# Optimization experiments

Measured on AMD Instinct MI355X. Metric: run time of the kernel, lower is better.

The kernel has to match this reference:

```python
import jax, jax.numpy as jnp
import numpy as np

HEADS = 8
GS = 16
C = 512
E = 512
SCALE = (E / HEADS) ** -0.5
PNAMES = ['sa_qkv_w','sa_qkv_b','sa_pa_w','sa_pa_b','sa_ln1_g','sa_ln1_b','sa_f1_w','sa_f1_b','sa_f2_w','sa_f2_b','sa_ln2_g','sa_ln2_b','sa_c1_w','sa_c1_b','sa_c2_w','sa_c2_b','sa_bn_g','sa_bn_b','ca_q_w','ca_q_b','ca_k_w','ca_k_b','ca_v_w','ca_v_b','ca_pa_w','ca_pa_b','p_q_w','p_q_b','p_k_w','p_k_b','p_v_w','p_v_b','p_pa_w','p_pa_b','p_ln_g','p_ln_b','p_lin_w','p_lin_b']


def _ln(x, g, b, eps=1e-5):
    m = x.mean(-1, keepdims=True)
    v = jnp.var(x, axis=-1, keepdims=True)
    return (x - m) / jnp.sqrt(v + eps) * g + b


def _conv1x1(x, w, b):
    return jnp.einsum('bchw,oc->bohw', x, w) + b[None, :, None, None]


def _up_ac(x, out=GS):
    # bilinear upsample, align_corners=True (nn.UpsamplingBilinear2d)
    H = x.shape[2]
    pos = jnp.arange(out) * (H - 1) / (out - 1)
    lo = jnp.floor(pos).astype(jnp.int32)
    hi = jnp.minimum(lo + 1, H - 1)
    w = (pos - lo).astype(x.dtype)
    xr = x[:, :, lo, :] * (1 - w)[None, None, :, None] + x[:, :, hi, :] * w[None, None, :, None]
    return xr[:, :, :, lo] * (1 - w) + xr[:, :, :, hi] * w


def _asri(x, p):
    # Sequence_ASRI: GAP tokens -> attention over the batch axis -> pixel-shuffle back
    B = x.shape[0]; ch = E // HEADS
    gap = x.mean((2, 3))                                             # [B,C]
    qkv = (gap @ p['sa_qkv_w'].T + p['sa_qkv_b']).reshape(B, 4, ch, HEADS).transpose(1, 3, 0, 2)  # [4,H,B,ch]
    q, k, v, skip = qkv[0], qkv[1], qkv[2], qkv[3]
    attn = jax.nn.softmax(jnp.einsum('hbc,hdc->hbd', q, k) * SCALE, -1)  # [H,B,B]
    o = jnp.einsum('hbd,hdc->hbc', attn, v)
    merge = lambda t: t.transpose(1, 2, 0).reshape(B, E)             # 'head b c -> b (c head)'
    a = merge(o) @ p['sa_pa_w'].T + p['sa_pa_b'] + merge(skip)
    h = jax.nn.relu(_ln(a, p['sa_ln1_g'], p['sa_ln1_b']) @ p['sa_f1_w'].T + p['sa_f1_b'])
    a = h @ p['sa_f2_w'].T + p['sa_f2_b'] + a
    s = _ln(a, p['sa_ln2_g'], p['sa_ln2_b']) @ p['sa_c1_w'].T + p['sa_c1_b']  # [B,C*16]
    s = _up_ac(s.reshape(B, C, 4, 4))                                 # pixel shuffle p1=p2=4 then bilinear to 16x16
    s = _conv1x1(s, p['sa_c2_w'], p['sa_c2_b'])
    # BatchNorm2d in eval mode (running_mean=0, running_var=1, eps=1e-5)
    s = s / np.float32(np.sqrt(1.0 + 1e-5)) * p['sa_bn_g'][None, :, None, None] + p['sa_bn_b'][None, :, None, None]
    return x + jax.nn.relu(s)


def _sscm(x1, x2, p):
    # Sequence_SSCM: GAP-token q/k over batch axis, full spatial v
    B = x1.shape[0]; ch = E // HEADS
    q = (x1.mean((2, 3)) @ p['ca_q_w'].T + p['ca_q_b']).reshape(B, ch, HEADS).transpose(2, 0, 1)  # [H,B,ch]
    k = (x2.mean((2, 3)) @ p['ca_k_w'].T + p['ca_k_b']).reshape(B, ch, HEADS).transpose(2, 0, 1)
    v = _conv1x1(x2, p['ca_v_w'], p['ca_v_b']).reshape(B, ch, HEADS, GS, GS).transpose(2, 0, 1, 3, 4).reshape(HEADS, B, ch * GS * GS)
    attn = jax.nn.softmax(jnp.einsum('hbc,hdc->hbd', q, k) * SCALE, -1)  # [H,B,B]
    o = jnp.einsum('hbd,hdm->hbm', attn, v)
    o = o.reshape(HEADS, B, ch, GS, GS).transpose(1, 2, 0, 3, 4).reshape(B, E, GS, GS)
    return jax.nn.relu(_conv1x1(o, p['ca_pa_w'], p['ca_pa_b']))


def _pixel(x1, x2, p):
    # Pixel_SSCM: pixel-wise cross-batch attention (no scale -- matches source)
    B = x1.shape[0]; ch = E // HEADS; N = GS * GS
    split = lambda t: t.reshape(B, ch, HEADS, N).transpose(2, 0, 3, 1)   # 'b (c head) h w -> head b (h w) c'
    q = split(_conv1x1(x1, p['p_q_w'], p['p_q_b']))                      # [H,B,N,ch]
    k = split(_conv1x1(x2, p['p_k_w'], p['p_k_b']))
    v = split(_conv1x1(x2, p['p_v_w'], p['p_v_b'])).reshape(HEADS, B * N, ch)
    attn = jax.nn.softmax(jnp.einsum('hbnc,hqmc->hbqnm', q, k), -1)      # [H,B,B,N,N]
    attn = attn.transpose(1, 0, 3, 2, 4).reshape(B, HEADS, N, B * N)     # 'head b q h w -> b head h (q w)'
    o = jnp.einsum('bhnm,hmc->bhnc', attn, v)
    o = o.transpose(0, 3, 1, 2).reshape(B, E, GS, GS)                    # 'b head (h w) c -> b (c head) h w'
    o = _conv1x1(o, p['p_pa_w'], p['p_pa_b']) + x1
    t = o.reshape(B, C, N).transpose(0, 2, 1)                            # [B,N,C]
    t = jax.nn.relu(_ln(t, p['p_ln_g'], p['p_ln_b']) @ p['p_lin_w'].T + p['p_lin_b'])
    return t.transpose(0, 2, 1).reshape(B, C, GS, GS)


def _hrlm(p, xs, xq):
    sa_s = _asri(xs, p)
    sa_q = _asri(xq, p)
    ca_s = _sscm(sa_s, sa_q, p)
    ca_q = _sscm(sa_q, sa_s, p)
    return _pixel(sa_s, ca_q, p), _pixel(sa_q, ca_s, p)


def setup_inputs():
    key = jax.random.key(0)
    ks = iter(jax.random.split(key, 64))
    w = lambda *s: (jax.random.normal(next(ks), s) * 0.02).astype(jnp.float32)
    z = lambda n: jnp.zeros((n,), jnp.float32)
    o = lambda n: jnp.ones((n,), jnp.float32)
    return dict(
        fea_support=jax.random.normal(next(ks), (8, C, GS, GS), jnp.float32),
        fea_query=jax.random.normal(next(ks), (8, C, GS, GS), jnp.float32),
        sa_qkv_w=w(4 * E, C), sa_qkv_b=z(4 * E),
        sa_pa_w=w(E, E), sa_pa_b=z(E),
        sa_ln1_g=o(E), sa_ln1_b=z(E),
        sa_f1_w=w(E, E), sa_f1_b=z(E), sa_f2_w=w(E, E), sa_f2_b=z(E),
        sa_ln2_g=o(E), sa_ln2_b=z(E),
        sa_c1_w=w(C * 16, E), sa_c1_b=z(C * 16),
        sa_c2_w=w(C, E), sa_c2_b=z(C),
        sa_bn_g=o(C), sa_bn_b=z(C),
        ca_q_w=w(E, C), ca_q_b=z(E), ca_k_w=w(E, C), ca_k_b=z(E),
        ca_v_w=w(E, C), ca_v_b=z(E), ca_pa_w=w(C, E), ca_pa_b=z(C),
        p_q_w=w(E, C), p_q_b=z(E), p_k_w=w(E, C), p_k_b=z(E),
        p_v_w=w(E, C), p_v_b=z(E), p_pa_w=w(C, E), p_pa_b=z(C),
        p_ln_g=o(C), p_ln_b=z(C), p_lin_w=w(C, C), p_lin_b=z(C),
    )


def reference(fea_support, fea_query, sa_qkv_w, sa_qkv_b, sa_pa_w, sa_pa_b, sa_ln1_g, sa_ln1_b, sa_f1_w, sa_f1_b, sa_f2_w, sa_f2_b, sa_ln2_g, sa_ln2_b, sa_c1_w, sa_c1_b, sa_c2_w, sa_c2_b, sa_bn_g, sa_bn_b, ca_q_w, ca_q_b, ca_k_w, ca_k_b, ca_v_w, ca_v_b, ca_pa_w, ca_pa_b, p_q_w, p_q_b, p_k_w, p_k_b, p_v_w, p_v_b, p_pa_w, p_pa_b, p_ln_g, p_ln_b, p_lin_w, p_lin_b):
    p = dict(zip(PNAMES, (sa_qkv_w, sa_qkv_b, sa_pa_w, sa_pa_b, sa_ln1_g, sa_ln1_b, sa_f1_w, sa_f1_b, sa_f2_w, sa_f2_b, sa_ln2_g, sa_ln2_b, sa_c1_w, sa_c1_b, sa_c2_w, sa_c2_b, sa_bn_g, sa_bn_b, ca_q_w, ca_q_b, ca_k_w, ca_k_b, ca_v_w, ca_v_b, ca_pa_w, ca_pa_b, p_q_w, p_q_b, p_k_w, p_k_b, p_v_w, p_v_b, p_pa_w, p_pa_b, p_ln_g, p_ln_b, p_lin_w, p_lin_b)))
    return _hrlm(p, fea_support, fea_query)
```

## Files before the change

### kernel.cpp

```cpp
#include <hip/hip_runtime.h>
#include <cmath>

#define IMG 131072
#define BIGF 1048576

#define CF_RELU  1
#define CF_RES   2
#define CF_BN    4
#define CF_SPLIT 8
#define CF_TRANS 16

typedef __attribute__((ext_vector_type(8))) short short8;
typedef __attribute__((ext_vector_type(4))) short short4v;
typedef __attribute__((ext_vector_type(4))) float f32x4;

__device__ __forceinline__ float wave_sum(float v){
    #pragma unroll
    for (int off = 32; off; off >>= 1) v += __shfl_xor(v, off);
    return v;
}

__device__ __forceinline__ unsigned short bf16_rn(float x){
    union { float f; unsigned u; } v; v.f = x;
    unsigned r = v.u + 0x7FFF + ((v.u >> 16) & 1);
    return (unsigned short)(r >> 16);
}
__device__ __forceinline__ float bf16_to_f(unsigned short h){
    union { float f; unsigned u; } v; v.u = ((unsigned)h) << 16;
    return v.f;
}
__device__ __forceinline__ unsigned pack_split(float x){
    unsigned short hi = bf16_rn(x);
    unsigned short lo = bf16_rn(x - bf16_to_f(hi));
    return (unsigned)hi | ((unsigned)lo << 16);
}
__device__ __forceinline__ unsigned pk_hi(unsigned a, unsigned b){
    return __builtin_amdgcn_perm(b, a, 0x05040100u);
}
__device__ __forceinline__ unsigned pk_lo(unsigned a, unsigned b){
    return __builtin_amdgcn_perm(b, a, 0x07060302u);
}

struct GapJobs  { const float* x[2]; float* o[2]; };
struct G8Job    { const float* in; const float* W; const float* bias; const float* add; float* out; };
struct G8Jobs   { G8Job j[4]; };
struct AAJobs   { const float* qkv[2]; float* om[2]; };
struct LnJobs   { const float* in[2]; float* out[2]; };
struct UpJobs   { const float* in[2]; float* out[2]; };
struct SAJobs   { const float* q8[2]; const float* k8[2]; float* aw[2]; };
struct SPJobs   { const float* aw[2]; const float* v[2]; float* out[2]; };
struct ZJobs    { float* p[2]; };
struct ConvJob  { const float* X; const float* X2; const float* W; const float* B; const float* R;
                  const float* bng; const float* bnb; float* O; int flags; };
struct ConvJobs { ConvJob j[6]; };
struct PixJob   { const unsigned* Q; const unsigned* K; const unsigned* V; float* Oa; float* Ob; };
struct PixJobs  { PixJob j[2]; };

__global__ __launch_bounds__(64) void k_gap(GapJobs jo){
    const int br = blockIdx.y;
    const int bc = blockIdx.x;
    const int lane = threadIdx.x;
    const float* p = jo.x[br] + (size_t)bc * 256;
    float s = p[lane] + p[lane + 64] + p[lane + 128] + p[lane + 192];
    s = wave_sum(s);
    if (lane == 0) jo.o[br][bc] = s * (1.0f / 256.0f);
}

__global__ __launch_bounds__(64) void k_gemm8(G8Jobs jo, int add_off, int add_stride, int O, int relu){
    const G8Job j = jo.j[blockIdx.y];
    const int o = blockIdx.x;
    const int lane = threadIdx.x;
    const float* wr = j.W + (size_t)o * 512;
    float acc[8] = {0,0,0,0,0,0,0,0};
    #pragma unroll
    for (int i = 0; i < 8; i++){
        float w = wr[lane + 64*i];
        #pragma unroll
        for (int b = 0; b < 8; b++) acc[b] += w * j.in[b*512 + lane + 64*i];
    }
    #pragma unroll
    for (int b = 0; b < 8; b++) acc[b] = wave_sum(acc[b]);
    if (lane < 8){
        float v = acc[0];
        #pragma unroll
        for (int b = 1; b < 8; b++) if (lane == b) v = acc[b];
        v += j.bias[o];
        if (j.add) v += j.add[lane*add_stride + add_off + o];
        if (relu) v = fmaxf(v, 0.f);
        j.out[(size_t)lane * O + o] = v;
    }
}

__global__ __launch_bounds__(64) void k_asri_attn(AAJobs jo){
    const int br = blockIdx.y;
    const float* qkv = jo.qkv[br];
    const int h = blockIdx.x >> 3, b = blockIdx.x & 7, c = threadIdx.x;
    const int ci = c*8 + h;
    float qc = qkv[b*2048 + ci];
    float s[8];
    #pragma unroll
    for (int d = 0; d < 8; d++){
        float p = qc * qkv[d*2048 + 512 + ci];
        p = wave_sum(p);
        s[d] = p * 0.125f;
    }
    float m = s[0];
    #pragma unroll
    for (int d = 1; d < 8; d++) m = fmaxf(m, s[d]);
    float sum = 0.f;
    #pragma unroll
    for (int d = 0; d < 8; d++){ s[d] = __expf(s[d]-m); sum += s[d]; }
    float r = 1.f / sum;
    float oc = 0.f;
    #pragma unroll
    for (int d = 0; d < 8; d++) oc += s[d]*r * qkv[d*2048 + 1024 + ci];
    jo.om[br][b*512 + ci] = oc;
}

__global__ __launch_bounds__(64) void k_ln8(LnJobs jo,
    const float* __restrict__ g, const float* __restrict__ be)
{
    const int br = blockIdx.y;
    const int b = blockIdx.x, lane = threadIdx.x;
    const float* in = jo.in[br];
    float v[8]; float s = 0.f;
    #pragma unroll
    for (int i = 0; i < 8; i++){ v[i] = in[b*512 + lane + 64*i]; s += v[i]; }
    s = wave_sum(s);
    float mean = s * (1.f/512.f);
    float q = 0.f;
    #pragma unroll
    for (int i = 0; i < 8; i++){ float d = v[i]-mean; q += d*d; }
    q = wave_sum(q);
    float rstd = rsqrtf(q*(1.f/512.f) + 1e-5f);
    #pragma unroll
    for (int i = 0; i < 8; i++){
        int c = lane + 64*i;
        jo.out[br][b*512 + c] = (v[i]-mean)*rstd*g[c] + be[c];
    }
}

__global__ __launch_bounds__(256) void k_up(UpJobs jo){
    const int br = blockIdx.y;
    const int idx = blockIdx.x*256 + threadIdx.x;
    const int x = idx & 15, y = (idx >> 4) & 15, bc = idx >> 8;
    float px = (float)(x*3) / 15.0f, py = (float)(y*3) / 15.0f;
    int lx = (int)px, ly = (int)py;
    float wx = px - lx, wy = py - ly;
    int hx = min(lx+1, 3), hy = min(ly+1, 3);
    const float* p = jo.in[br] + (size_t)bc * 16;
    float v00 = p[ly*4+lx], v01 = p[ly*4+hx], v10 = p[hy*4+lx], v11 = p[hy*4+hx];
    float a0 = v00*(1.f-wy) + v10*wy;
    float a1 = v01*(1.f-wy) + v11*wy;
    jo.out[br][idx] = a0*(1.f-wx) + a1*wx;
}

__global__ __launch_bounds__(256) void k_zero(ZJobs jo){
    jo.p[blockIdx.y][(size_t)blockIdx.x*256 + threadIdx.x] = 0.f;
}

#define LDK 40
__device__ __forceinline__ void convm_body(
    const float* __restrict__ Xb, const float* __restrict__ X2b,
    const float* __restrict__ W,
    const float* __restrict__ bias, const float* __restrict__ resb,
    const float* __restrict__ bng, const float* __restrict__ bnb, float bninv,
    float* __restrict__ outb, int flags, int o0, int n0, unsigned short* lds)
{
    const int tid512 = threadIdx.x;
    const int g   = tid512 >> 8;
    const int tid = tid512 & 255;
    unsigned short* sAh = lds + g*10240;
    unsigned short* sAl = sAh + 2560;
    unsigned short* sBh = sAl + 2560;
    unsigned short* sBl = sBh + 2560;
    const int wv = tid >> 6, lane = tid & 63;
    const int quad = lane >> 4, l16 = lane & 15;
    const int wo = (wv >> 1) * 32, wn = (wv & 1) * 32;
    const int so  = tid >> 2, sk8 = (tid & 3) * 8;
    const int sp  = tid & 15, sn  = (tid >> 4) * 4;

    const bool trans = (flags & CF_TRANS) != 0;
    int so_g = o0 + so;
    if (trans) so_g = ((so_g & 63) << 3) | (so_g >> 6);

    const float* wrow = W + (size_t)so_g*512 + g*256 + sk8;
    const size_t xoff = (size_t)(g*256 + 2*sp)*256 + n0 + sn;
    const float* xrow  = Xb + xoff;
    const float* x2row = X2b ? X2b + xoff : nullptr;

    auto ldx4 = [&](size_t off){
        float4 v = *(const float4*)(xrow + off);
        if (x2row){
            float4 w2 = *(const float4*)(x2row + off);
            v.x += w2.x; v.y += w2.y; v.z += w2.z; v.w += w2.w;
        }
        return v;
    };

    f32x4 acc[2][2] = {};
    float4 a0 = *(const float4*)(wrow);
    float4 a1 = *(const float4*)(wrow + 4);
    float4 x0 = ldx4(0);
    float4 x1 = ldx4(256);

    for (int k0 = 0; k0 < 256; k0 += 32){
        __syncthreads();
        {
            float wa[8] = {a0.x,a0.y,a0.z,a0.w,a1.x,a1.y,a1.z,a1.w};
            #pragma unroll
            for (int j = 0; j < 4; j++){
                unsigned short h0 = bf16_rn(wa[2*j]);
                unsigned short h1 = bf16_rn(wa[2*j+1]);
                unsigned short g0 = bf16_rn(wa[2*j]   - bf16_to_f(h0));
                unsigned short g1 = bf16_rn(wa[2*j+1] - bf16_to_f(h1));
                *(unsigned*)&sAh[so*LDK + sk8 + 2*j] = (unsigned)h0 | ((unsigned)h1 << 16);
                *(unsigned*)&sAl[so*LDK + sk8 + 2*j] = (unsigned)g0 | ((unsigned)g1 << 16);
            }
            float xe[4] = {x0.x,x0.y,x0.z,x0.w};
            float xo[4] = {x1.x,x1.y,x1.z,x1.w};
            #pragma unroll
            for (int j = 0; j < 4; j++){
                unsigned short h0 = bf16_rn(xe[j]);
                unsigned short h1 = bf16_rn(xo[j]);
                unsigned short g0 = bf16_rn(xe[j] - bf16_to_f(h0));
                unsigned short g1 = bf16_rn(xo[j] - bf16_to_f(h1));
                *(unsigned*)&sBh[(sn+j)*LDK + 2*sp] = (unsigned)h0 | ((unsigned)h1 << 16);
                *(unsigned*)&sBl[(sn+j)*LDK + 2*sp] = (unsigned)g0 | ((unsigned)g1 << 16);
            }
        }
        __syncthreads();
        if (k0 + 32 < 256){
            a0 = *(const float4*)(wrow + k0 + 32);
            a1 = *(const float4*)(wrow + k0 + 36);
            x0 = ldx4((size_t)(k0+32)*256);
            x1 = ldx4((size_t)(k0+32)*256 + 256);
        }
        short8 ah[2], al[2], bh[2], bl[2];
        #pragma unroll
        for (int t = 0; t < 2; t++){
            int ai = (wo + 16*t + l16)*LDK + quad*8;
            ah[t] = *(const short8*)&sAh[ai];
            al[t] = *(const short8*)&sAl[ai];
            int bi = (wn + 16*t + l16)*LDK + quad*8;
            bh[t] = *(const short8*)&sBh[bi];
            bl[t] = *(const short8*)&sBl[bi];
        }
        if (trans){
            #pragma unroll
            for (int mt = 0; mt < 2; mt++){
                #pragma unroll
                for (int nt = 0; nt < 2; nt++){
                    acc[mt][nt] = __builtin_amdgcn_mfma_f32_16x16x32_bf16(bh[nt], ah[mt], acc[mt][nt], 0, 0, 0);
                    acc[mt][nt] = __builtin_amdgcn_mfma_f32_16x16x32_bf16(bl[nt], ah[mt], acc[mt][nt], 0, 0, 0);
                    acc[mt][nt] = __builtin_amdgcn_mfma_f32_16x16x32_bf16(bh[nt], al[mt], acc[mt][nt], 0, 0, 0);
                }
            }
        } else {
            #pragma unroll
            for (int mt = 0; mt < 2; mt++){
                #pragma unroll
                for (int nt = 0; nt < 2; nt++){
                    acc[mt][nt] = __builtin_amdgcn_mfma_f32_16x16x32_bf16(ah[mt], bh[nt], acc[mt][nt], 0, 0, 0);
                    acc[mt][nt] = __builtin_amdgcn_mfma_f32_16x16x32_bf16(ah[mt], bl[nt], acc[mt][nt], 0, 0, 0);
                    acc[mt][nt] = __builtin_amdgcn_mfma_f32_16x16x32_bf16(al[mt], bh[nt], acc[mt][nt], 0, 0, 0);
                }
            }
        }
    }
    __syncthreads();
    float* red = (float*)lds;
    if (g == 1){
        float* r = red + tid*20;
        #pragma unroll
        for (int mt = 0; mt < 2; mt++)
            #pragma unroll
            for (int nt = 0; nt < 2; nt++)
                *(f32x4*)(r + (mt*2+nt)*4) = acc[mt][nt];
    }
    __syncthreads();
    if (g == 0){
        float* r = red + tid*20;
        #pragma unroll
        for (int mt = 0; mt < 2; mt++)
            #pragma unroll
            for (int nt = 0; nt < 2; nt++){
                f32x4 o4 = *(const f32x4*)(r + (mt*2+nt)*4);
                acc[mt][nt] += o4;
            }
        if (trans){
            unsigned* op = (unsigned*)outb;
            #pragma unroll
            for (int mt = 0; mt < 2; mt++){
                #pragma unroll
                for (int nt = 0; nt < 2; nt++){
                    const int p  = o0 + wo + 16*mt + l16;
                    const int nb = n0 + wn + 16*nt + quad*4;
                    const int osrc = ((p & 63) << 3) | (p >> 6);
                    const float bs = bias[osrc];
                    #pragma unroll
                    for (int rr = 0; rr < 4; rr++){
                        float v = acc[mt][nt][rr] + bs;
                        op[(size_t)(nb+rr)*512 + p] = pack_split(v);
                    }
                }
            }
        } else {
            #pragma unroll
            for (int mt = 0; mt < 2; mt++){
                #pragma unroll
                for (int nt = 0; nt < 2; nt++){
                    const int n  = n0 + wn + 16*nt + l16;
                    const int ob = o0 + wo + 16*mt + quad*4;
                    #pragma unroll
                    for (int rr = 0; rr < 4; rr++){
                        const int o = ob + rr;
                        float v = acc[mt][nt][rr] + bias[o];
                        if (flags & CF_BN)   v = v*(bninv*bng[o]) + bnb[o];
                        if (flags & CF_RELU) v = fmaxf(v, 0.f);
                        if (flags & CF_RES)  v += resb[(size_t)o*256 + n];
                        if (flags & CF_SPLIT){
                            ((unsigned*)outb)[(size_t)o*256 + n] = pack_split(v);
                        } else {
                            outb[(size_t)o*256 + n] = v;
                        }
                    }
                }
            }
        }
    }
}

__global__ __launch_bounds__(512) void k_convm(ConvJobs jo, float bninv)
{
    __shared__ unsigned short lds[20480];
    const int z = blockIdx.z;
    const ConvJob j = jo.j[z >> 3];
    const int b = z & 7;
    convm_body(j.X + (size_t)b*IMG,
               j.X2 ? j.X2 + (size_t)b*IMG : nullptr,
               j.W, j.B,
               j.R ? j.R + (size_t)b*IMG : nullptr,
               j.bng, j.bnb, bninv,
               j.O + (size_t)b*IMG, j.flags,
               blockIdx.y*64, blockIdx.x*64, lds);
}

__global__ __launch_bounds__(64) void k_sscm_attn(SAJobs jo)
{
    const int br = blockIdx.y;
    const int h = blockIdx.x >> 3, b = blockIdx.x & 7, c = threadIdx.x;
    const int ci = c*8 + h;
    float qc = jo.q8[br][b*512 + ci];
    float s[8];
    #pragma unroll
    for (int d = 0; d < 8; d++){
        float p = qc * jo.k8[br][d*512 + ci];
        p = wave_sum(p);
        s[d] = p * 0.125f;
    }
    float m = s[0];
    #pragma unroll
    for (int d = 1; d < 8; d++) m = fmaxf(m, s[d]);
    float sum = 0.f;
    #pragma unroll
    for (int d = 0; d < 8; d++){ s[d] = __expf(s[d]-m); sum += s[d]; }
    float r = 1.f/sum;
    if (c < 8){
        float v = s[0];
        #pragma unroll
        for (int d = 1; d < 8; d++) if (c == d) v = s[d];
        jo.aw[br][blockIdx.x*8 + c] = v*r;
    }
}

__global__ __launch_bounds__(256) void k_sscm_apply(SPJobs jo)
{
    const int br = blockIdx.y;
    const int idx = blockIdx.x*256 + threadIdx.x;
    const int pix = idx & 255, e = (idx >> 8) & 511, b = idx >> 17;
    const int h = e & 7;
    const float* aw = jo.aw[br] + (h*8 + b)*8;
    const float* v = jo.v[br];
    float acc = 0.f;
    #pragma unroll
    for (int d = 0; d < 8; d++) acc += aw[d] * v[(size_t)d*IMG + (size_t)e*256 + pix];
    jo.out[br][idx] = acc;
}

__global__ __launch_bounds__(256) void k_pixel_mfma(PixJobs jo)
{
    __shared__ char smem[40960];
    unsigned short* sQh = (unsigned short*)smem;
    unsigned short* sQl = sQh + 2*64*40;
    unsigned short* sKh = sQl + 2*64*40;
    unsigned short* sKl = sKh + 2*64*40;
    unsigned short* sP  = (unsigned short*)smem;
    unsigned short* sVh = sKh;
    unsigned short* sVl = sKl;

    const int br = blockIdx.y >> 3, b = blockIdx.y & 7;
    const PixJob J = jo.j[br];
    const int nt = blockIdx.x & 3, dg = blockIdx.x >> 2;
    const int h = blockIdx.z;
    const int tid = threadIdx.x;
    const int wv = tid >> 6, lane = tid & 63;
    const int quad = lane >> 4, l16 = lane & 15;
    const int n0 = nt * 64;

    {
        const unsigned* Qt = J.Q + (size_t)b*IMG + (size_t)n0*512 + h*64;
        const int q = tid >> 2, i0 = (tid & 3) * 16;
        const unsigned* src = Qt + (size_t)q*512 + i0;
        uint4 w0 = *(const uint4*)(src);
        uint4 w1 = *(const uint4*)(src + 4);
        uint4 w2 = *(const uint4*)(src + 8);
        uint4 w3 = *(const uint4*)(src + 12);
        unsigned hb[8], lb[8];
        hb[0]=pk_hi(w0.x,w0.y); hb[1]=pk_hi(w0.z,w0.w); hb[2]=pk_hi(w1.x,w1.y); hb[3]=pk_hi(w1.z,w1.w);
        hb[4]=pk_hi(w2.x,w2.y); hb[5]=pk_hi(w2.z,w2.w); hb[6]=pk_hi(w3.x,w3.y); hb[7]=pk_hi(w3.z,w3.w);
        lb[0]=pk_lo(w0.x,w0.y); lb[1]=pk_lo(w0.z,w0.w); lb[2]=pk_lo(w1.x,w1.y); lb[3]=pk_lo(w1.z,w1.w);
        lb[4]=pk_lo(w2.x,w2.y); lb[5]=pk_lo(w2.z,w2.w); lb[6]=pk_lo(w3.x,w3.y); lb[7]=pk_lo(w3.z,w3.w);
        int dst = (i0>>5)*2560 + q*40 + (i0&31);
        *(uint4*)&sQh[dst]     = *(uint4*)&hb[0];
        *(uint4*)&sQh[dst + 8] = *(uint4*)&hb[4];
        *(uint4*)&sQl[dst]     = *(uint4*)&lb[0];
        *(uint4*)&sQl[dst + 8] = *(uint4*)&lb[4];
    }
    __syncthreads();

    short8 bqh[2], bql[2];
    #pragma unroll
    for (int ks = 0; ks < 2; ks++){
        int idx = ks*2560 + (wv*16 + l16)*40 + quad*8;
        bqh[ks] = *(const short8*)&sQh[idx];
        bql[ks] = *(const short8*)&sQl[idx];
    }

    f32x4 oac[4] = {};

    for (int dd = 0; dd < 4; dd++){
        const int d = dg*4 + dd;

        f32x4 S[16] = {};
        #pragma unroll
        for (int mq = 0; mq < 4; mq++){
            if (mq | dd) __syncthreads();
            {
                const unsigned* Kt = J.K + (size_t)d*IMG + (size_t)(mq*64)*512 + h*64;
                const int mloc = tid & 63, cb0 = tid >> 6;
                #pragma unroll
                for (int p = 0; p < 2; p++){
                    int cb = cb0 + 4*p;
                    const unsigned* src = Kt + (size_t)mloc*512 + cb*8;
                    uint4 wa = *(const uint4*)(src);
                    uint4 wb = *(const uint4*)(src + 4);
                    union { short8 s; unsigned u[4]; } hu, lu;
                    hu.u[0]=pk_hi(wa.x,wa.y); hu.u[1]=pk_hi(wa.z,wa.w);
                    hu.u[2]=pk_hi(wb.x,wb.y); hu.u[3]=pk_hi(wb.z,wb.w);
                    lu.u[0]=pk_lo(wa.x,wa.y); lu.u[1]=pk_lo(wa.z,wa.w);
                    lu.u[2]=pk_lo(wb.x,wb.y); lu.u[3]=pk_lo(wb.z,wb.w);
                    int idx = (cb>>2)*2560 + mloc*40 + (cb&3)*8;
                    *(short8*)&sKh[idx] = hu.s;
                    *(short8*)&sKl[idx] = lu.s;
                }
            }
            __syncthreads();
            #pragma unroll
            for (int mtl = 0; mtl < 4; mtl++){
                int t = mq*4 + mtl;
                #pragma unroll
                for (int ks = 0; ks < 2; ks++){
                    int idx = ks*2560 + (mtl*16 + l16)*40 + quad*8;
                    short8 ah = *(const short8*)&sKh[idx];
                    short8 al = *(const short8*)&sKl[idx];
                    S[t] = __builtin_amdgcn_mfma_f32_16x16x32_bf16(ah, bqh[ks], S[t], 0, 0, 0);
                    S[t] = __builtin_amdgcn_mfma_f32_16x16x32_bf16(ah, bql[ks], S[t], 0, 0, 0);
                    S[t] = __builtin_amdgcn_mfma_f32_16x16x32_bf16(al, bqh[ks], S[t], 0, 0, 0);
                }
            }
        }

        {
            float mx = -3.4e38f;
            #pragma unroll
            for (int t = 0; t < 16; t++)
                #pragma unroll
                for (int r = 0; r < 4; r++) mx = fmaxf(mx, S[t][r]);
            mx = fmaxf(mx, __shfl_xor(mx, 16));
            mx = fmaxf(mx, __shfl_xor(mx, 32));
            float sum = 0.f;
            #pragma unroll
            for (int t = 0; t < 16; t++)
                #pragma unroll
                for (int r = 0; r < 4; r++){ S[t][r] = __expf(S[t][r]-mx); sum += S[t][r]; }
            sum += __shfl_xor(sum, 16);
            sum += __shfl_xor(sum, 32);
            float rr = 1.f/sum;
            #pragma unroll
            for (int t = 0; t < 16; t++)
                #pragma unroll
                for (int r = 0; r < 4; r++) S[t][r] *= rr;
        }

        #pragma unroll
        for (int hm = 0; hm < 2; hm++){
            __syncthreads();
            #pragma unroll
            for (int mtl = 0; mtl < 8; mtl++){
                int t = hm*8 + mtl;
                short4v p4;
                #pragma unroll
                for (int r = 0; r < 4; r++) p4[r] = (short)bf16_rn(S[t][r]);
                int idx = (mtl>>1)*2560 + (wv*16 + l16)*40 + 16*(mtl&1) + quad*4;
                *(short4v*)&sP[idx] = p4;
            }
            #pragma unroll
            for (int sub = 0; sub < 2; sub++){
                if (sub) __syncthreads();
                {
                    const unsigned* Vp = J.V + (size_t)d*IMG + (size_t)h*256 + hm*128 + sub*64;
                    const int mp = tid & 31, c0 = tid >> 5;
                    #pragma unroll
                    for (int p = 0; p < 8; p++){
                        int c = c0 + 8*p;
                        const unsigned* src = Vp + (size_t)c*2048 + 2*mp;
                        uint2 w = *(const uint2*)(src);
                        int idx = ((2*mp)>>5)*2560 + c*40 + ((2*mp)&31);
                        *(unsigned*)&sVh[idx] = pk_hi(w.x, w.y);
                        *(unsigned*)&sVl[idx] = pk_lo(w.x, w.y);
                    }
                }
                __syncthreads();
                #pragma unroll
                for (int l = 0; l < 2; l++){
                    int gks = sub*2 + l;
                    int pidx = gks*2560 + (wv*16 + l16)*40 + quad*8;
                    short8 bp = *(const short8*)&sP[pidx];
                    #pragma unroll
                    for (int ct = 0; ct < 4; ct++){
                        int vidx = l*2560 + (ct*16 + l16)*40 + quad*8;
                        short8 vh = *(const short8*)&sVh[vidx];
                        short8 vl = *(const short8*)&sVl[vidx];
                        oac[ct] = __builtin_amdgcn_mfma_f32_16x16x32_bf16(vh, bp, oac[ct], 0, 0, 0);
                        oac[ct] = __builtin_amdgcn_mfma_f32_16x16x32_bf16(vl, bp, oac[ct], 0, 0, 0);
                    }
                }
            }
        }
    }

    {
        float* base = (J.Ob ? (dg ? J.Ob : J.Oa) : J.Oa);
        float* Obp = base + (size_t)b * IMG;
        const int q = n0 + wv*16 + l16;
        if (J.Ob){
            #pragma unroll
            for (int ct = 0; ct < 4; ct++){
                #pragma unroll
                for (int r = 0; r < 4; r++){
                    int c = ct*16 + quad*4 + r;
                    Obp[(size_t)(c*8+h)*256 + q] = oac[ct][r];
                }
            }
        } else {
            #pragma unroll
            for (int ct = 0; ct < 4; ct++){
                #pragma unroll
                for (int r = 0; r < 4; r++){
                    int c = ct*16 + quad*4 + r;
                    unsafeAtomicAdd(&Obp[(size_t)(c*8+h)*256 + q], oac[ct][r]);
                }
            }
        }
    }
}

__global__ __launch_bounds__(64) void k_ln_pix(LnJobs jo,
    const float* __restrict__ g, const float* __restrict__ be)
{
    const int br = blockIdx.y;
    const int bn = blockIdx.x;
    const int b = bn >> 8, n = bn & 255;
    const int lane = threadIdx.x;
    const float* p = jo.in[br] + (size_t)b*IMG + n;
    float v[8]; float s = 0.f;
    #pragma unroll
    for (int i = 0; i < 8; i++){ v[i] = p[(size_t)(lane + 64*i)*256]; s += v[i]; }
    s = wave_sum(s);
    float mean = s * (1.f/512.f);
    float q = 0.f;
    #pragma unroll
    for (int i = 0; i < 8; i++){ float d = v[i]-mean; q += d*d; }
    q = wave_sum(q);
    float rstd = rsqrtf(q*(1.f/512.f) + 1e-5f);
    #pragma unroll
    for (int i = 0; i < 8; i++){
        int c = lane + 64*i;
        jo.out[br][(size_t)b*IMG + (size_t)c*256 + n] = (v[i]-mean)*rstd*g[c] + be[c];
    }
}

extern "C" void kernel_launch(void* const* d_in, const int* in_sizes, int n_in,
                              void* d_out, int out_size, void* d_ws, size_t ws_size,
                              hipStream_t stream)
{
    const float* xs    = (const float*)d_in[0];
    const float* xq    = (const float*)d_in[1];
    const float* qkvw  = (const float*)d_in[2];  const float* qkvb = (const float*)d_in[3];
    const float* paw   = (const float*)d_in[4];  const float* pab  = (const float*)d_in[5];
    const float* ln1g  = (const float*)d_in[6];  const float* ln1b = (const float*)d_in[7];
    const float* f1w   = (const float*)d_in[8];  const float* f1b  = (const float*)d_in[9];
    const float* f2w   = (const float*)d_in[10]; const float* f2b  = (const float*)d_in[11];
    const float* ln2g  = (const float*)d_in[12]; const float* ln2b = (const float*)d_in[13];
    const float* c1w   = (const float*)d_in[14]; const float* c1b  = (const float*)d_in[15];
    const float* c2w   = (const float*)d_in[16]; const float* c2b  = (const float*)d_in[17];
    const float* bng   = (const float*)d_in[18]; const float* bnb  = (const float*)d_in[19];
    const float* caqw  = (const float*)d_in[20]; const float* caqb = (const float*)d_in[21];
    const float* cakw  = (const float*)d_in[22]; const float* cakb = (const float*)d_in[23];
    const float* cavw  = (const float*)d_in[24]; const float* cavb = (const float*)d_in[25];
    const float* capw  = (const float*)d_in[26]; const float* capb = (const float*)d_in[27];
    const float* pqw   = (const float*)d_in[28]; const float* pqb  = (const float*)d_in[29];
    const float* pkw   = (const float*)d_in[30]; const float* pkb  = (const float*)d_in[31];
    const float* pvw   = (const float*)d_in[32]; const float* pvb  = (const float*)d_in[33];
    const float* ppw   = (const float*)d_in[34]; const float* ppb  = (const float*)d_in[35];
    const float* plng  = (const float*)d_in[36]; const float* plnb = (const float*)d_in[37];
    const float* plinw = (const float*)d_in[38]; const float* plinb= (const float*)d_in[39];

    const size_t SMF = 262144;
    float* ws = (float*)d_ws;
    float* smb = ws;
    float* B[14];
    for (int i = 0; i < 14; i++) B[i] = ws + SMF + (size_t)i*BIGF;
    float* sa_s = B[0]; float* sa_q = B[1];
    float* ca_s = B[2]; float* ca_q = B[3];
    const bool paired_pixel = ws_size >= (SMF + 12*(size_t)BIGF)*sizeof(float) + 1024;
    const bool has_dsplit   = ws_size >= (SMF + 14*(size_t)BIGF)*sizeof(float) + 1024;

    auto SM = [&](int br){ return smb + (size_t)br*131072; };
    auto GAP=[&](int br){ return SM(br); };            auto QKV=[&](int br){ return SM(br)+4096; };
    auto OM =[&](int br){ return SM(br)+20480; };      auto AA =[&](int br){ return SM(br)+24576; };
    auto HB =[&](int br){ return SM(br)+28672; };      auto A2 =[&](int br){ return SM(br)+32768; };
    auto LNB=[&](int br){ return SM(br)+36864; };      auto S8 =[&](int br){ return SM(br)+40960; };
    auto ATW=[&](int br){ return SM(br)+106496; };     auto Q8 =[&](int br){ return SM(br)+107008; };
    auto K8 =[&](int br){ return SM(br)+111104; };

    const float bninv = 1.0f / sqrtf(1.0f + 1e-5f);
    float* out0 = (float*)d_out;
    float* out1 = out0 + (size_t)BIGF;

    {
        GapJobs gj = {{xs, xq}, {GAP(0), GAP(1)}};
        k_gap<<<dim3(4096,2), 64, 0, stream>>>(gj);
        G8Jobs qj = {{{GAP(0), qkvw, qkvb, nullptr, QKV(0)}, {GAP(1), qkvw, qkvb, nullptr, QKV(1)}}};
        k_gemm8<<<dim3(2048,2), 64, 0, stream>>>(qj, 0, 0, 2048, 0);
        AAJobs aj = {{QKV(0), QKV(1)}, {OM(0), OM(1)}};
        k_asri_attn<<<dim3(64,2), 64, 0, stream>>>(aj);
        G8Jobs pj = {{{OM(0), paw, pab, QKV(0), AA(0)}, {OM(1), paw, pab, QKV(1), AA(1)}}};
        k_gemm8<<<dim3(512,2), 64, 0, stream>>>(pj, 1536, 2048, 512, 0);
        LnJobs l1 = {{AA(0), AA(1)}, {LNB(0), LNB(1)}};
        k_ln8<<<dim3(8,2), 64, 0, stream>>>(l1, ln1g, ln1b);
        G8Jobs fj = {{{LNB(0), f1w, f1b, nullptr, HB(0)}, {LNB(1), f1w, f1b, nullptr, HB(1)}}};
        k_gemm8<<<dim3(512,2), 64, 0, stream>>>(fj, 0, 0, 512, 1);
        G8Jobs f2j = {{{HB(0), f2w, f2b, AA(0), A2(0)}, {HB(1), f2w, f2b, AA(1), A2(1)}}};
        k_gemm8<<<dim3(512,2), 64, 0, stream>>>(f2j, 0, 512, 512, 0);
        LnJobs l2 = {{A2(0), A2(1)}, {LNB(0), LNB(1)}};
        k_ln8<<<dim3(8,2), 64, 0, stream>>>(l2, ln2g, ln2b);
        G8Jobs cj = {{{LNB(0), c1w, c1b, nullptr, S8(0)}, {LNB(1), c1w, c1b, nullptr, S8(1)}}};
        k_gemm8<<<dim3(8192,2), 64, 0, stream>>>(cj, 0, 0, 8192, 0);
        UpJobs uj = {{S8(0), S8(1)}, {B[4], B[5]}};
        k_up<<<dim3(4096,2), 256, 0, stream>>>(uj);
        ConvJobs c2j = {};
        c2j.j[0] = {B[4], nullptr, c2w, c2b, xs, bng, bnb, sa_s, CF_BN|CF_RELU|CF_RES};
        c2j.j[1] = {B[5], nullptr, c2w, c2b, xq, bng, bnb, sa_q, CF_BN|CF_RELU|CF_RES};
        k_convm<<<dim3(4,8,16), 512, 0, stream>>>(c2j, bninv);
    }

    {
        GapJobs gj = {{sa_s, sa_q}, {GAP(0), GAP(1)}};
        k_gap<<<dim3(4096,2), 64, 0, stream>>>(gj);
        G8Jobs qj = {{{GAP(0), caqw, caqb, nullptr, Q8(0)},
                      {GAP(1), cakw, cakb, nullptr, K8(0)},
                      {GAP(1), caqw, caqb, nullptr, Q8(1)},
                      {GAP(0), cakw, cakb, nullptr, K8(1)}}};
        k_gemm8<<<dim3(512,4), 64, 0, stream>>>(qj, 0, 0, 512, 0);
        SAJobs sj = {{Q8(0), Q8(1)}, {K8(0), K8(1)}, {ATW(0), ATW(1)}};
        k_sscm_attn<<<dim3(64,2), 64, 0, stream>>>(sj);
        ConvJobs vj = {};
        vj.j[0] = {sa_q, nullptr, cavw, cavb, nullptr, nullptr, nullptr, B[4], 0};
        vj.j[1] = {sa_s, nullptr, cavw, cavb, nullptr, nullptr, nullptr, B[5], 0};
        k_convm<<<dim3(4,8,16), 512, 0, stream>>>(vj, 1.f);
        SPJobs pj = {{ATW(0), ATW(1)}, {B[4], B[5]}, {B[6], B[7]}};
        k_sscm_apply<<<dim3(4096,2), 256, 0, stream>>>(pj);
        ConvJobs aj = {};
        aj.j[0] = {B[6], nullptr, capw, capb, nullptr, nullptr, nullptr, ca_s, CF_RELU};
        aj.j[1] = {B[7], nullptr, capw, capb, nullptr, nullptr, nullptr, ca_q, CF_RELU};
        k_convm<<<dim3(4,8,16), 512, 0, stream>>>(aj, 1.f);
    }

    if (paired_pixel){
        ConvJobs qkvj = {};
        qkvj.j[0] = {sa_s, nullptr, pqw, pqb, nullptr, nullptr, nullptr, B[4],  CF_SPLIT|CF_TRANS};
        qkvj.j[1] = {ca_q, nullptr, pkw, pkb, nullptr, nullptr, nullptr, B[5],  CF_SPLIT|CF_TRANS};
        qkvj.j[2] = {ca_q, nullptr, pvw, pvb, nullptr, nullptr, nullptr, B[6],  CF_SPLIT};
        qkvj.j[3] = {sa_q, nullptr, pqw, pqb, nullptr, nullptr, nullptr, B[8],  CF_SPLIT|CF_TRANS};
        qkvj.j[4] = {ca_s, nullptr, pkw, pkb, nullptr, nullptr, nullptr, B[9],  CF_SPLIT|CF_TRANS};
        qkvj.j[5] = {ca_s, nullptr, pvw, pvb, nullptr, nullptr, nullptr, B[10], CF_SPLIT};
        k_convm<<<dim3(4,8,48), 512, 0, stream>>>(qkvj, 1.f);
        if (!has_dsplit){
            ZJobs zj = {{B[7], B[11]}};
            k_zero<<<dim3(4096,2), 256, 0, stream>>>(zj);
        }
        float* o2a = has_dsplit ? B[12] : nullptr;
        float* o2b = has_dsplit ? B[13] : nullptr;
        PixJobs pxj = {{{(const unsigned*)B[4], (const unsigned*)B[5], (const unsigned*)B[6],  B[7],  o2a},
                        {(const unsigned*)B[8], (const unsigned*)B[9], (const unsigned*)B[10], B[11], o2b}}};
        k_pixel_mfma<<<dim3(8,16,8), 256, 0, stream>>>(pxj);
        ConvJobs ppj = {};
        ppj.j[0] = {B[7],  o2a, ppw, ppb, sa_s, nullptr, nullptr, out0, CF_RES};
        ppj.j[1] = {B[11], o2b, ppw, ppb, sa_q, nullptr, nullptr, out1, CF_RES};
        k_convm<<<dim3(4,8,16), 512, 0, stream>>>(ppj, 1.f);
        LnJobs lj = {{out0, out1}, {B[4], B[8]}};
        k_ln_pix<<<dim3(2048,2), 64, 0, stream>>>(lj, plng, plnb);
        ConvJobs lnj = {};
        lnj.j[0] = {B[4], nullptr, plinw, plinb, nullptr, nullptr, nullptr, out0, CF_RELU};
        lnj.j[1] = {B[8], nullptr, plinw, plinb, nullptr, nullptr, nullptr, out1, CF_RELU};
        k_convm<<<dim3(4,8,16), 512, 0, stream>>>(lnj, 1.f);
    } else {
        auto pixel1 = [&](const float* x1, const float* x2, float* out){
            ConvJobs qkvj = {};
            qkvj.j[0] = {x1, nullptr, pqw, pqb, nullptr, nullptr, nullptr, B[4], CF_SPLIT|CF_TRANS};
            qkvj.j[1] = {x2, nullptr, pkw, pkb, nullptr, nullptr, nullptr, B[5], CF_SPLIT|CF_TRANS};
            qkvj.j[2] = {x2, nullptr, pvw, pvb, nullptr, nullptr, nullptr, B[6], CF_SPLIT};
            k_convm<<<dim3(4,8,24), 512, 0, stream>>>(qkvj, 1.f);
            ZJobs zj = {{B[7], B[7]}};
            k_zero<<<dim3(4096,1), 256, 0, stream>>>(zj);
            PixJobs pxj = {{{(const unsigned*)B[4], (const unsigned*)B[5], (const unsigned*)B[6], B[7], nullptr},
                            {(const unsigned*)B[4], (const unsigned*)B[5], (const unsigned*)B[6], B[7], nullptr}}};
            k_pixel_mfma<<<dim3(8,8,8), 256, 0, stream>>>(pxj);
            ConvJobs ppj = {};
            ppj.j[0] = {B[7], nullptr, ppw, ppb, x1, nullptr, nullptr, out, CF_RES};
            k_convm<<<dim3(4,8,8), 512, 0, stream>>>(ppj, 1.f);
            LnJobs lj = {{out, out}, {B[4], B[4]}};
            k_ln_pix<<<dim3(2048,1), 64, 0, stream>>>(lj, plng, plnb);
            ConvJobs lnj = {};
            lnj.j[0] = {B[4], nullptr, plinw, plinb, nullptr, nullptr, nullptr, out, CF_RELU};
            k_convm<<<dim3(4,8,8), 512, 0, stream>>>(lnj, 1.f);
        };
        pixel1(sa_s, ca_q, out0);
        pixel1(sa_q, ca_s, out1);
    }

    (void)in_sizes; (void)n_in; (void)out_size;
}
```

Before: 488.1 us.

## Register-prefetch K and V tiles across attention loop stages

Global loads of the next K or V tile now go into registers before the current tile's MFMA work, and are written to shared memory at the start of the next stage. The V loop is flattened into four stages so prefetching chains across K→V→next-d K. s_setprio raises wave priority around the MFMA blocks. The intent is to hide global load latency behind matrix math, at the cost of more live registers that may lower occupancy.

```diff
diff --git a/kernel.cpp b/kernel.cpp
--- a/kernel.cpp
+++ b/kernel.cpp
@@ -437,7 +437,55 @@
         bql[ks] = *(const short8*)&sQl[idx];
     }
 
+    const int mloc = tid & 63, cb0 = tid >> 6;
+    const int mp = tid & 31,  c0v = tid >> 5;
+    uint4 pf[4];
+
+    auto loadK = [&](int d, int mq){
+        const unsigned* Kt = J.K + (size_t)d*IMG + (size_t)(mq*64 + mloc)*512 + h*64;
+        pf[0] = *(const uint4*)(Kt + cb0*8);
+        pf[1] = *(const uint4*)(Kt + cb0*8 + 4);
+        pf[2] = *(const uint4*)(Kt + (cb0+4)*8);
+        pf[3] = *(const uint4*)(Kt + (cb0+4)*8 + 4);
+    };
+    auto writeK = [&](){
+        #pragma unroll
+        for (int p = 0; p < 2; p++){
+            uint4 wa = pf[2*p], wb = pf[2*p+1];
+            union { short8 s; unsigned u[4]; } hu, lu;
+            hu.u[0]=pk_hi(wa.x,wa.y); hu.u[1]=pk_hi(wa.z,wa.w);
+            hu.u[2]=pk_hi(wb.x,wb.y); hu.u[3]=pk_hi(wb.z,wb.w);
+            lu.u[0]=pk_lo(wa.x,wa.y); lu.u[1]=pk_lo(wa.z,wa.w);
+            lu.u[2]=pk_lo(wb.x,wb.y); lu.u[3]=pk_lo(wb.z,wb.w);
+            int cb = cb0 + 4*p;
+            int idx = (cb>>2)*2560 + mloc*40 + (cb&3)*8;
+            *(short8*)&sKh[idx] = hu.s;
+            *(short8*)&sKl[idx] = lu.s;
+        }
+    };
+    auto loadV = [&](int d, int vs){
+        const unsigned* Vp = J.V + (size_t)d*IMG + (size_t)h*256 + (vs>>1)*128 + (vs&1)*64 + 2*mp;
+        #pragma unroll
+        for (int p2 = 0; p2 < 4; p2++){
+            uint2 wA = *(const uint2*)(Vp + (size_t)(c0v + 16*p2)*2048);
+            uint2 wB = *(const uint2*)(Vp + (size_t)(c0v + 16*p2 + 8)*2048);
+            pf[p2].x = wA.x; pf[p2].y = wA.y; pf[p2].z = wB.x; pf[p2].w = wB.y;
+        }
+    };
+    auto writeV = [&](){
+        const int ib = ((2*mp)>>5)*2560 + ((2*mp)&31);
+        #pragma unroll
+        for (int p2 = 0; p2 < 4; p2++){
+            int ca = c0v + 16*p2, cb2 = ca + 8;
+            *(unsigned*)&sVh[ib + ca*40]  = pk_hi(pf[p2].x, pf[p2].y);
+            *(unsigned*)&sVl[ib + ca*40]  = pk_lo(pf[p2].x, pf[p2].y);
+            *(unsigned*)&sVh[ib + cb2*40] = pk_hi(pf[p2].z, pf[p2].w);
+            *(unsigned*)&sVl[ib + cb2*40] = pk_lo(pf[p2].z, pf[p2].w);
+        }
+    };
+
     f32x4 oac[4] = {};
+    loadK(dg*4, 0);
 
     for (int dd = 0; dd < 4; dd++){
         const int d = dg*4 + dd;
@@ -446,26 +494,11 @@
         #pragma unroll
         for (int mq = 0; mq < 4; mq++){
             if (mq | dd) __syncthreads();
-            {
-                const unsigned* Kt = J.K + (size_t)d*IMG + (size_t)(mq*64)*512 + h*64;
-                const int mloc = tid & 63, cb0 = tid >> 6;
-                #pragma unroll
-                for (int p = 0; p < 2; p++){
-                    int cb = cb0 + 4*p;
-                    const unsigned* src = Kt + (size_t)mloc*512 + cb*8;
-                    uint4 wa = *(const uint4*)(src);
-                    uint4 wb = *(const uint4*)(src + 4);
-                    union { short8 s; unsigned u[4]; } hu, lu;
-                    hu.u[0]=pk_hi(wa.x,wa.y); hu.u[1]=pk_hi(wa.z,wa.w);
-                    hu.u[2]=pk_hi(wb.x,wb.y); hu.u[3]=pk_hi(wb.z,wb.w);
-                    lu.u[0]=pk_lo(wa.x,wa.y); lu.u[1]=pk_lo(wa.z,wa.w);
-                    lu.u[2]=pk_lo(wb.x,wb.y); lu.u[3]=pk_lo(wb.z,wb.w);
-                    int idx = (cb>>2)*2560 + mloc*40 + (cb&3)*8;
-                    *(short8*)&sKh[idx] = hu.s;
-                    *(short8*)&sKl[idx] = lu.s;
-                }
-            }
+            writeK();
+            if (mq < 3) loadK(d, mq+1);
+            else        loadV(d, 0);
             __syncthreads();
+            __builtin_amdgcn_s_setprio(1);
             #pragma unroll
             for (int mtl = 0; mtl < 4; mtl++){
                 int t = mq*4 + mtl;
@@ -479,6 +512,7 @@
                     S[t] = __builtin_amdgcn_mfma_f32_16x16x32_bf16(al, bqh[ks], S[t], 0, 0, 0);
                 }
             }
+            __builtin_amdgcn_s_setprio(0);
         }
 
         {
@@ -504,49 +538,40 @@
         }
 
         #pragma unroll
-        for (int hm = 0; hm < 2; hm++){
+        for (int vs = 0; vs < 4; vs++){
             __syncthreads();
-            #pragma unroll
-            for (int mtl = 0; mtl < 8; mtl++){
-                int t = hm*8 + mtl;
-                short4v p4;
-                #pragma unroll
-                for (int r = 0; r < 4; r++) p4[r] = (short)bf16_rn(S[t][r]);
-                int idx = (mtl>>1)*2560 + (wv*16 + l16)*40 + 16*(mtl&1) + quad*4;
-                *(short4v*)&sP[idx] = p4;
-            }
-            #pragma unroll
-            for (int sub = 0; sub < 2; sub++){
-                if (sub) __syncthreads();
-                {
-                    const unsigned* Vp = J.V + (size_t)d*IMG + (size_t)h*256 + hm*128 + sub*64;
-                    const int mp = tid & 31, c0 = tid >> 5;
+            if ((vs & 1) == 0){
+                const int hm = vs >> 1;
+                #pragma unroll
+                for (int mtl = 0; mtl < 8; mtl++){
+                    int t = hm*8 + mtl;
+                    short4v p4;
                     #pragma unroll
-                    for (int p = 0; p < 8; p++){
-                        int c = c0 + 8*p;
-                        const unsigned* src = Vp + (size_t)c*2048 + 2*mp;
-                        uint2 w = *(const uint2*)(src);
-                        int idx = ((2*mp)>>5)*2560 + c*40 + ((2*mp)&31);
-                        *(unsigned*)&sVh[idx] = pk_hi(w.x, w.y);
-                        *(unsigned*)&sVl[idx] = pk_lo(w.x, w.y);
-                    }
-                }
-                __syncthreads();
-                #pragma unroll
-                for (int l = 0; l < 2; l++){
-                    int gks = sub*2 + l;
-                    int pidx = gks*2560 + (wv*16 + l16)*40 + quad*8;
-                    short8 bp = *(const short8*)&sP[pidx];
-                    #pragma unroll
-                    for (int ct = 0; ct < 4; ct++){
-                        int vidx = l*2560 + (ct*16 + l16)*40 + quad*8;
-                        short8 vh = *(const short8*)&sVh[vidx];
-                        short8 vl = *(const short8*)&sVl[vidx];
-                        oac[ct] = __builtin_amdgcn_mfma_f32_16x16x32_bf16(vh, bp, oac[ct], 0, 0, 0);
-                        oac[ct] = __builtin_amdgcn_mfma_f32_16x16x32_bf16(vl, bp, oac[ct], 0, 0, 0);
-                    }
-                }
-            }
+                    for (int r = 0; r < 4; r++) p4[r] = (short)bf16_rn(S[t][r]);
+                    int idx = (mtl>>1)*2560 + (wv*16 + l16)*40 + 16*(mtl&1) + quad*4;
+                    *(short4v*)&sP[idx] = p4;
+                }
+            }
+            writeV();
+            if (vs < 3)      loadV(d, vs+1);
+            else if (dd < 3) loadK(d+1, 0);
+            __syncthreads();
+            __builtin_amdgcn_s_setprio(1);
+            #pragma unroll
+            for (int l = 0; l < 2; l++){
+                int gks = (vs & 1)*2 + l;
+                int pidx = gks*2560 + (wv*16 + l16)*40 + quad*8;
+                short8 bp = *(const short8*)&sP[pidx];
+                #pragma unroll
+                for (int ct = 0; ct < 4; ct++){
+                    int vidx = l*2560 + (ct*16 + l16)*40 + quad*8;
+                    short8 vh = *(const short8*)&sVh[vidx];
+                    short8 vl = *(const short8*)&sVl[vidx];
+                    oac[ct] = __builtin_amdgcn_mfma_f32_16x16x32_bf16(vh, bp, oac[ct], 0, 0, 0);
+                    oac[ct] = __builtin_amdgcn_mfma_f32_16x16x32_bf16(vl, bp, oac[ct], 0, 0, 0);
+                }
+            }
+            __builtin_amdgcn_s_setprio(0);
         }
     }
 
```

Measured after the change: 473.5 us, median of 3. -3.0%, faster.
